# Performance work log

Hardware: AMD Instinct MI355X
Metric: run time of the kernel (lower is better)

## Reference

```python
import jax, jax.numpy as jnp
import numpy as np

T_MIN, T_MAX = 0.6, 1.6
SIM_LO, SIM_HI = 0.5, 0.9
LN_EPS = 1e-5


def _layernorm(x, gamma, beta):
    mu = jnp.mean(x, axis=-1, keepdims=True)
    var = jnp.mean((x - mu) ** 2, axis=-1, keepdims=True)
    return (x - mu) * jax.lax.rsqrt(var + LN_EPS) * gamma + beta


def _cos_sim(a, b, eps=1e-8):
    num = jnp.sum(a * b, axis=-1)
    na = jnp.maximum(jnp.sqrt(jnp.sum(a * a, axis=-1)), eps)
    nb = jnp.maximum(jnp.sqrt(jnp.sum(b * b, axis=-1)), eps)
    return num / (na * nb)


def setup_inputs() -> dict:
    key = jax.random.key(0)
    B, L, D = 2, 4096, 512
    ks = jax.random.split(key, 10)
    s = 0.02
    return {
        "x": jax.random.normal(ks[0], (B, L, D), dtype=jnp.float32),
        "Wq": jax.random.normal(ks[1], (D, D), dtype=jnp.float32) * s,
        "Wk": jax.random.normal(ks[2], (D, D), dtype=jnp.float32) * s,
        "Wv": jax.random.normal(ks[3], (D, D), dtype=jnp.float32) * s,
        "Wp": jax.random.normal(ks[4], (D, D), dtype=jnp.float32) * s,
        "W1": jax.random.normal(ks[5], (4 * D, D), dtype=jnp.float32) * s,
        "b1": jnp.zeros((4 * D,), dtype=jnp.float32),
        "W2": jax.random.normal(ks[6], (D, 4 * D), dtype=jnp.float32) * s,
        "b2": jnp.zeros((D,), dtype=jnp.float32),
        "gamma": jnp.ones((D,), dtype=jnp.float32),
        "beta": jnp.zeros((D,), dtype=jnp.float32),
    }


def reference(x, Wq, Wk, Wv, Wp, W1, b1, W2, b2, gamma, beta):
    B, L, D = x.shape
    xn = _layernorm(x, gamma, beta)
    # TinyAttn with T=1.0, causal=True (torch Linear: x @ W.T)
    Q = jnp.einsum("bld,ed->ble", xn, Wq)
    K = jnp.einsum("bld,ed->ble", xn, Wk)
    V = jnp.einsum("bld,ed->ble", xn, Wv)
    scores = jnp.einsum("bld,bmd->blm", Q, K) / jnp.sqrt(jnp.asarray(D, x.dtype))
    causal = jnp.triu(jnp.ones((L, L), dtype=bool), 1)
    scores = jnp.where(causal, jnp.asarray(-1e30, x.dtype), scores)
    attn = jax.nn.softmax(scores, axis=-1)  # [B, L, L]
    out = jnp.einsum("blm,bmd->bld", attn, V)
    out = jnp.einsum("bld,ed->ble", out, Wp)
    ctx = x + out
    h = _layernorm(ctx, gamma, beta)
    h = jax.nn.gelu(jnp.einsum("bld,fd->blf", h, W1) + b1, approximate=False)
    ctx = ctx + jnp.einsum("blf,df->bld", h, W2) + b2

    # AdaptiveController on last-token attention row
    last_attn = attn[:, -1]  # [B, L]
    p = jnp.clip(last_attn, 1e-9, None)
    H = -jnp.sum(p * jnp.log(p), axis=-1)  # [B]
    Hn = (H - H.min()) / (H.max() - H.min() + 1e-9)
    Hm = jax.lax.stop_gradient(jnp.mean(Hn))  # detached in torch
    T = T_MIN + (T_MAX - T_MIN) * Hm
    sim_th = SIM_HI - (SIM_HI - SIM_LO) * Hm

    # UnconsciousStack: single forward -> stack holds only the just-pushed (K, V), detached.
    q_vec = jnp.mean(Q[:, -1], axis=0, keepdims=True)  # [1, D]
    K_rep = jax.lax.stop_gradient(jnp.mean(K, axis=1))  # [B, D]
    s = jnp.mean(_cos_sim(q_vec, K_rep))  # scalar
    hit = s >= sim_th

    K_cat = jnp.concatenate([K, jax.lax.stop_gradient(K)], axis=1)  # [B, 2L, D]
    V_cat = jnp.concatenate([V, jax.lax.stop_gradient(V)], axis=1)
    scores2 = jnp.einsum("bld,bmd->blm", Q, K_cat) / jnp.sqrt(jnp.asarray(D, x.dtype))
    attn2 = jax.nn.softmax(scores2 / T, axis=-1)  # [B, L, 2L], no causal mask
    reatt = jnp.einsum("blm,bmd->bld", attn2, V_cat)
    ctx = ctx + jnp.where(hit, reatt, jnp.zeros_like(reatt))
    return ctx
```

## Files before the change

kernel.cpp:

```cpp
#include <hip/hip_runtime.h>
#include <math.h>

#define BATCH 2
#define SEQ 4096
#define DIM 512
#define FF 2048
#define NROWS (BATCH*SEQ)
#define KT 32
#define RSQRT_D 0.044194173824159216f

typedef __attribute__((ext_vector_type(8))) short short8;
typedef __attribute__((ext_vector_type(4))) short short4v;
typedef __attribute__((ext_vector_type(4))) float f32x4;

__device__ __forceinline__ float gelu_f(float v) {
    return 0.5f * v * (1.0f + erff(v * 0.70710678118654752440f));
}
__device__ __forceinline__ short bf16b(float x) {
    union { float f; unsigned u; } c; c.f = x;
    unsigned r = (c.u + 0x7FFFu + ((c.u >> 16) & 1u)) >> 16;
    return (short)r;
}
__device__ __forceinline__ float bf16f(short h) {
    union { unsigned u; float f; } c; c.u = ((unsigned)(unsigned short)h) << 16;
    return c.f;
}
__device__ __forceinline__ void gload16(const void* g, void* l) {
    __builtin_amdgcn_global_load_lds(
        (const __attribute__((address_space(1))) unsigned int*)g,
        (__attribute__((address_space(3))) unsigned int*)l, 16, 0, 0);
}
__device__ __forceinline__ float blk_sum256(float v, volatile float* sm) {
    #pragma unroll
    for (int o = 32; o; o >>= 1) v += __shfl_xor(v, o);
    __syncthreads();
    if ((threadIdx.x & 63) == 0) sm[threadIdx.x >> 6] = v;
    __syncthreads();
    return sm[0] + sm[1] + sm[2] + sm[3];
}

__global__ __launch_bounds__(256) void f2bf_all(
        const float* __restrict__ Wq, const float* __restrict__ Wk,
        const float* __restrict__ Wv, const float* __restrict__ Wp,
        const float* __restrict__ W1, const float* __restrict__ W2,
        short* __restrict__ Wcat, short* __restrict__ Wpb,
        short* __restrict__ W1b, short* __restrict__ W2b)
{
    int i = blockIdx.x * 256 + threadIdx.x;
    const float* src; short* dst; int loc;
    if      (i <  32768) { src = Wq; dst = Wcat;          loc = i; }
    else if (i <  65536) { src = Wk; dst = Wcat + 262144; loc = i - 32768; }
    else if (i <  98304) { src = Wv; dst = Wcat + 524288; loc = i - 65536; }
    else if (i < 131072) { src = Wp; dst = Wpb;           loc = i - 98304; }
    else if (i < 262144) { src = W1; dst = W1b;           loc = i - 131072; }
    else                 { src = W2; dst = W2b;           loc = i - 262144; }
    const float4* p = (const float4*)(src + (size_t)loc * 8);
    float4 a = p[0], b = p[1];
    short8 r;
    r[0]=bf16b(a.x); r[1]=bf16b(a.y); r[2]=bf16b(a.z); r[3]=bf16b(a.w);
    r[4]=bf16b(b.x); r[5]=bf16b(b.y); r[6]=bf16b(b.z); r[7]=bf16b(b.w);
    *(short8*)(dst + (size_t)loc * 8) = r;
}

__global__ __launch_bounds__(256) void ln_kernel(const float* __restrict__ x,
        const float* __restrict__ g, const float* __restrict__ be,
        short* __restrict__ o)
{
    int row  = blockIdx.x * 4 + (threadIdx.x >> 6);
    int lane = threadIdx.x & 63;
    const float4* xr = (const float4*)(x + (size_t)row * DIM);
    float4 v0 = xr[lane*2], v1 = xr[lane*2+1];
    float s = v0.x+v0.y+v0.z+v0.w + v1.x+v1.y+v1.z+v1.w;
    #pragma unroll
    for (int off = 32; off; off >>= 1) s += __shfl_xor(s, off);
    float mu = s * (1.0f/DIM);
    float d[8] = {v0.x-mu, v0.y-mu, v0.z-mu, v0.w-mu, v1.x-mu, v1.y-mu, v1.z-mu, v1.w-mu};
    float q = 0.f;
    #pragma unroll
    for (int j = 0; j < 8; ++j) q += d[j]*d[j];
    #pragma unroll
    for (int off = 32; off; off >>= 1) q += __shfl_xor(q, off);
    float rs = rsqrtf(q * (1.0f/DIM) + 1e-5f);
    const float4* g4 = (const float4*)g;
    const float4* b4 = (const float4*)be;
    float4 ga = g4[lane*2], gb = g4[lane*2+1];
    float4 ba = b4[lane*2], bb = b4[lane*2+1];
    float gv[8] = {ga.x,ga.y,ga.z,ga.w, gb.x,gb.y,gb.z,gb.w};
    float bv[8] = {ba.x,ba.y,ba.z,ba.w, bb.x,bb.y,bb.z,bb.w};
    short8 r;
    #pragma unroll
    for (int j = 0; j < 8; ++j) r[j] = bf16b(d[j]*rs*gv[j] + bv[j]);
    *(short8*)(o + (size_t)row * DIM + lane*8) = r;
}

__global__ __launch_bounds__(256) void gemm_v2(
        const short* __restrict__ A, const short* __restrict__ W,
        const float* __restrict__ bias, const float* __restrict__ res,
        float* __restrict__ Cf, short* __restrict__ Cb,
        short* __restrict__ CbK, short* __restrict__ CbV,
        int K, int sa, int sw, int sc, int act, int accum)
{
    __shared__ short As[2][4096];
    __shared__ short Ws[2][4096];
    int tid = threadIdx.x;
    int m0 = blockIdx.y * 128, n0 = blockIdx.x * 128;
    int w = tid >> 6, lane = tid & 63;
    int wr = (w >> 1) * 64, wc = (w & 1) * 64;
    int lr = lane & 15, lg = lane >> 4;
    int srow = tid >> 2, skoff = (tid & 3) * 8;
    const short* Ab = A + (size_t)(m0 + srow) * sa + skoff;
    const short* Wb = W + (size_t)(n0 + srow) * sw + skoff;

    #define STAGE_G(buf, kk) do { \
        gload16(Ab + (kk),                    As[buf] + tid*8); \
        gload16(Ab + (size_t)64*sa + (kk),    As[buf] + 2048 + tid*8); \
        gload16(Wb + (kk),                    Ws[buf] + tid*8); \
        gload16(Wb + (size_t)64*sw + (kk),    Ws[buf] + 2048 + tid*8); } while(0)

    f32x4 acc[4][4];
    f32x4 zero = {0.f, 0.f, 0.f, 0.f};
    #pragma unroll
    for (int i = 0; i < 4; ++i)
        #pragma unroll
        for (int j = 0; j < 4; ++j) acc[i][j] = zero;

    STAGE_G(0, 0);
    __syncthreads();
    int cur = 0;
    for (int k0 = 0; k0 < K; k0 += 32) {
        if (k0 + 32 < K) STAGE_G(cur ^ 1, k0 + 32);
        short8 a[4], b[4];
        #pragma unroll
        for (int i = 0; i < 4; ++i) a[i] = *(const short8*)(As[cur] + (wr + i*16 + lr)*32 + lg*8);
        #pragma unroll
        for (int j = 0; j < 4; ++j) b[j] = *(const short8*)(Ws[cur] + (wc + j*16 + lr)*32 + lg*8);
        #pragma unroll
        for (int i = 0; i < 4; ++i)
            #pragma unroll
            for (int j = 0; j < 4; ++j)
                acc[i][j] = __builtin_amdgcn_mfma_f32_16x16x32_bf16(a[i], b[j], acc[i][j], 0, 0, 0);
        __syncthreads();
        cur ^= 1;
    }
    #undef STAGE_G

    #pragma unroll
    for (int i = 0; i < 4; ++i) {
        #pragma unroll
        for (int r = 0; r < 4; ++r) {
            size_t m = (size_t)m0 + wr + i*16 + lg*4 + r;
            #pragma unroll
            for (int j = 0; j < 4; ++j) {
                int n = n0 + wc + j*16 + lr;
                float v = acc[i][j][r];
                if (bias) v += bias[n];
                if (act)  v = gelu_f(v);
                if (CbK) {
                    int seg = n >> 9, nl = n & 511;
                    short* dst = (seg == 0) ? Cb : (seg == 1) ? CbK : CbV;
                    dst[m * 512 + nl] = bf16b(v);
                } else {
                    if (res) v += res[m * sc + n];
                    size_t idx = m * sc + n;
                    if (Cf) { if (accum) Cf[idx] += v; else Cf[idx] = v; }
                    if (Cb) Cb[idx] = bf16b(v);
                }
            }
        }
    }
}

__global__ __launch_bounds__(256) void vtrans(const short* __restrict__ V,
                                              short* __restrict__ Vt)
{
    __shared__ short t_s[64][72];
    int l0 = blockIdx.x * 64, d0 = blockIdx.y * 64, b = blockIdx.z;
    int t = threadIdx.x;
    const short* src = V + (size_t)b * SEQ * DIM;
    #pragma unroll
    for (int it = 0; it < 2; ++it) {
        int r = (t >> 3) + it * 32, c = (t & 7) * 8;
        *(short8*)&t_s[r][c] = *(const short8*)(src + (size_t)(l0 + r) * DIM + d0 + c);
    }
    __syncthreads();
    short* dst = Vt + (size_t)b * DIM * SEQ;
    #pragma unroll
    for (int it = 0; it < 2; ++it) {
        int r = (t >> 3) + it * 32, c = (t & 7) * 8;
        short8 v;
        #pragma unroll
        for (int j = 0; j < 8; ++j) v[j] = t_s[c + j][r];
        *(short8*)(dst + (size_t)(d0 + r) * SEQ + l0 + c) = v;
    }
}

__global__ __launch_bounds__(512, 2) void attn_v4(
        const short* __restrict__ Q, const short* __restrict__ K,
        const short* __restrict__ Vt, short* __restrict__ Opart,
        float* __restrict__ Mpart, float* __restrict__ Lpart,
        float scale, const float* __restrict__ scale_ptr,
        const float* __restrict__ gate, int causal)
{
    if (gate && gate[0] == 0.0f) return;
    if (scale_ptr) scale = scale_ptr[0];
    extern __shared__ short lds[];
    short* k_s = lds;
    short* v_s = lds + 32768;
    short* p_s = lds + 65536;

    int tid = threadIdx.x, w = tid >> 6, lane = tid & 63;
    int rg = w >> 1, dh = w & 1;
    int lr = lane & 15, lg = lane >> 4;

    int bid = blockIdx.x;
    int cb = bid & 7;
    int c  = cb & 3, b = cb >> 2;
    int ip = bid >> 3;
    int jj0 = ip, jj1 = 63 - ip;
    int TA = causal ? 2*(ip+1)  : 128;
    int TB = causal ? 2*(64-ip) : 128;
    int Ttot = TA + TB;
    int s0 = (Ttot * c) >> 2, s1 = (Ttot * (c+1)) >> 2;

    size_t bofs = (size_t)b * SEQ * DIM;
    size_t vofs = (size_t)b * DIM * SEQ;
    f32x4 zero = {0.f, 0.f, 0.f, 0.f};

    for (int sg = 0; sg < 2; ++sg) {
        int j  = sg ? jj1 : jj0;
        int ta = sg ? (max(s0, TA) - TA) : s0;
        int tb = sg ? (s1 - TA)          : min(s1, TA);
        if (ta >= tb) continue;
        int qw0 = j*64 + rg*16;

        short8 qf[16];
        #pragma unroll
        for (int kc = 0; kc < 16; ++kc)
            qf[kc] = *(const short8*)(Q + bofs + (size_t)(qw0 + lr)*DIM + kc*32 + lg*8);

        f32x4 o[16];
        #pragma unroll
        for (int df = 0; df < 16; ++df) o[df] = zero;
        float mreg[4] = {-1e30f,-1e30f,-1e30f,-1e30f};
        float lreg[4] = {0.f,0.f,0.f,0.f};
        int rowg[4];
        #pragma unroll
        for (int r = 0; r < 4; ++r) rowg[r] = qw0 + lg*4 + r;

        int cur = 0;
        {
            int k0s = ta * KT;
            #pragma unroll
            for (int s4 = 0; s4 < 4; ++s4) {
                int slot = tid + s4*512;
                int row = slot >> 6, cg = slot & 63;
                gload16(K + bofs + (size_t)(k0s + row)*DIM + ((cg ^ (row & 7)) << 3),
                        k_s + slot*8);
                int dpair = slot >> 3, low = slot & 7;
                int d = dpair*2 + (low & 1);
                int kg = (low >> 1) ^ (dpair & 3);
                gload16(Vt + vofs + (size_t)d*SEQ + k0s + kg*8,
                        v_s + slot*8);
            }
        }
        __syncthreads();

        for (int t = ta; t < tb; ++t) {
            int k0 = t * KT;
            if (t + 1 < tb) {
                int k0s = (t + 1) * KT;
                int bo = (cur ^ 1) * 16384;
                #pragma unroll
                for (int s4 = 0; s4 < 4; ++s4) {
                    int slot = tid + s4*512;
                    int row = slot >> 6, cg = slot & 63;
                    gload16(K + bofs + (size_t)(k0s + row)*DIM + ((cg ^ (row & 7)) << 3),
                            k_s + bo + slot*8);
                    int dpair = slot >> 3, low = slot & 7;
                    int d = dpair*2 + (low & 1);
                    int kg = (low >> 1) ^ (dpair & 3);
                    gload16(Vt + vofs + (size_t)d*SEQ + k0s + kg*8,
                            v_s + bo + slot*8);
                }
            }
            f32x4 ss[2];
            ss[0] = zero; ss[1] = zero;
            const short* kb = k_s + cur*16384;
            #pragma unroll
            for (int kc = 0; kc < 16; ++kc) {
                #pragma unroll
                for (int kf = 0; kf < 2; ++kf) {
                    int row = kf*16 + lr;
                    short8 kk = *(const short8*)(kb + row*512 + (((kc*4 + lg) ^ (row & 7)) << 3));
                    ss[kf] = __builtin_amdgcn_mfma_f32_16x16x32_bf16(qf[kc], kk, ss[kf], 0, 0, 0);
                }
            }
            bool needmask = causal && (k0 + KT - 1 > qw0);
            #pragma unroll
            for (int kf = 0; kf < 2; ++kf) {
                int key = k0 + kf*16 + lr;
                #pragma unroll
                for (int r = 0; r < 4; ++r) {
                    float sv = ss[kf][r] * scale;
                    if (needmask && key > rowg[r]) sv = -1e30f;
                    ss[kf][r] = sv;
                }
            }
            float pm[4];
            bool tg = false;
            #pragma unroll
            for (int r = 0; r < 4; ++r) {
                pm[r] = fmaxf(ss[0][r], ss[1][r]);
                tg |= (pm[r] > mreg[r]);
            }
            if (__any(tg)) {
                #pragma unroll
                for (int r = 0; r < 4; ++r) {
                    float v = pm[r];
                    v = fmaxf(v, __shfl_xor(v, 1));
                    v = fmaxf(v, __shfl_xor(v, 2));
                    v = fmaxf(v, __shfl_xor(v, 4));
                    v = fmaxf(v, __shfl_xor(v, 8));
                    float nm = fmaxf(mreg[r], v);
                    float fr = __expf(mreg[r] - nm);
                    mreg[r] = nm;
                    lreg[r] *= fr;
                    #pragma unroll
                    for (int df = 0; df < 16; ++df) o[df][r] *= fr;
                }
            }
            #pragma unroll
            for (int kf = 0; kf < 2; ++kf) {
                #pragma unroll
                for (int r = 0; r < 4; ++r) {
                    float sv = ss[kf][r];
                    float p = (sv < -1e29f) ? 0.0f : __expf(sv - mreg[r]);
                    lreg[r] += p;
                    p_s[w*512 + (lg*4 + r)*32 + kf*16 + lr] = bf16b(p);
                }
            }
            short8 pa = *(const short8*)(p_s + w*512 + lr*32 + lg*8);
            const short* vb = v_s + cur*16384;
            #pragma unroll
            for (int df = 0; df < 16; ++df) {
                int d = dh*256 + df*16 + lr;
                int slot16 = (d >> 1)*8 + (((lg ^ ((d >> 1) & 3)) << 1) | (d & 1));
                short8 vv = *(const short8*)(vb + slot16*8);
                o[df] = __builtin_amdgcn_mfma_f32_16x16x32_bf16(pa, vv, o[df], 0, 0, 0);
            }
            __syncthreads();
            cur ^= 1;
        }

        #pragma unroll
        for (int r = 0; r < 4; ++r) {
            float v = lreg[r];
            v += __shfl_xor(v, 1);
            v += __shfl_xor(v, 2);
            v += __shfl_xor(v, 4);
            v += __shfl_xor(v, 8);
            lreg[r] = v;
        }
        int slot = (b*64 + j)*4 + c;
        size_t obase = ((size_t)slot*8 + w) * 4096;
        #pragma unroll
        for (int df = 0; df < 16; ++df) {
            short4v pk;
            #pragma unroll
            for (int r = 0; r < 4; ++r) pk[r] = bf16b(o[df][r]);
            *(short4v*)(Opart + obase + df*256 + lane*4) = pk;
        }
        if (dh == 0 && lr == 0) {
            #pragma unroll
            for (int r = 0; r < 4; ++r) {
                Mpart[slot*64 + rg*16 + lg*4 + r] = mreg[r];
                Lpart[slot*64 + rg*16 + lg*4 + r] = lreg[r];
            }
        }
    }
}

__global__ __launch_bounds__(256) void attn_merge(
        const short* __restrict__ Opart, const float* __restrict__ Mpart,
        const float* __restrict__ Lpart, short* __restrict__ attb,
        float* __restrict__ outf, const float* __restrict__ gate, int causal)
{
    if (gate && gate[0] == 0.0f) return;
    __shared__ float wts[4][64];
    int j = blockIdx.x, dh = blockIdx.y, b = blockIdx.z;
    int tid = threadIdx.x;
    int ip = (j < 32) ? j : 63 - j;
    int TA = causal ? 2*(ip+1)  : 128;
    int TB = causal ? 2*(64-ip) : 128;
    int Ttot = TA + TB;
    int jstart = (j < 32) ? 0 : TA;
    int jend   = (j < 32) ? TA : Ttot;
    bool val[4];
    #pragma unroll
    for (int c = 0; c < 4; ++c) {
        int sc = (Ttot * c) >> 2, ec = (Ttot * (c+1)) >> 2;
        val[c] = (sc < jend) && (ec > jstart);
    }
    if (tid < 64) {
        float M = -1e30f;
        #pragma unroll
        for (int c = 0; c < 4; ++c)
            if (val[c]) M = fmaxf(M, Mpart[((b*64 + j)*4 + c)*64 + tid]);
        float L = 0.f;
        #pragma unroll
        for (int c = 0; c < 4; ++c)
            if (val[c]) L += Lpart[((b*64 + j)*4 + c)*64 + tid]
                           * __expf(Mpart[((b*64 + j)*4 + c)*64 + tid] - M);
        float invL = 1.0f / L;
        #pragma unroll
        for (int c = 0; c < 4; ++c)
            wts[c][tid] = val[c]
                ? __expf(Mpart[((b*64 + j)*4 + c)*64 + tid] - M) * invL : 0.0f;
    }
    __syncthreads();
    int wv = tid >> 6, lane = tid & 63, lg = lane >> 4, lr = lane & 15;
    int region = wv*2 + dh;
    #pragma unroll 4
    for (int df = 0; df < 16; ++df) {
        float acc[4] = {0.f, 0.f, 0.f, 0.f};
        #pragma unroll
        for (int c = 0; c < 4; ++c) {
            if (!val[c]) continue;
            size_t idx = ((size_t)((b*64 + j)*4 + c)*8 + region)*4096 + df*256 + lane*4;
            short4v v = *(const short4v*)(Opart + idx);
            #pragma unroll
            for (int r = 0; r < 4; ++r)
                acc[r] += wts[c][wv*16 + lg*4 + r] * bf16f(v[r]);
        }
        #pragma unroll
        for (int r = 0; r < 4; ++r) {
            int row = j*64 + wv*16 + lg*4 + r;
            int d = dh*256 + df*16 + lr;
            size_t oidx = (size_t)b*SEQ*DIM + (size_t)row*DIM + d;
            if (attb) attb[oidx] = bf16b(acc[r]);
            else      outf[oidx] += acc[r];
        }
    }
}

__global__ __launch_bounds__(256) void lastrow_scores(const short* __restrict__ Q,
        const short* __restrict__ K, float* __restrict__ slast)
{
    __shared__ float q_l[DIM];
    int b = blockIdx.y;
    int m = blockIdx.x * 256 + threadIdx.x;
    for (int i = threadIdx.x; i < DIM; i += 256)
        q_l[i] = bf16f(Q[((size_t)b*SEQ + SEQ-1)*DIM + i]);
    __syncthreads();
    const short* kr = K + ((size_t)b*SEQ + m) * DIM;
    float s = 0.f;
    for (int d = 0; d < DIM; d += 8) {
        short8 k8 = *(const short8*)(kr + d);
        #pragma unroll
        for (int j = 0; j < 8; ++j) s += q_l[d + j] * bf16f(k8[j]);
    }
    slast[(size_t)b*SEQ + m] = s * RSQRT_D;
}

__global__ __launch_bounds__(256) void entropy_kernel(const float* __restrict__ slast,
        float* __restrict__ H)
{
    __shared__ float sm[4];
    int b = blockIdx.x, t = threadIdx.x;
    const float* s = slast + (size_t)b * SEQ;
    float v[16];
    float mx = -1e30f;
    #pragma unroll
    for (int j = 0; j < 16; ++j) { v[j] = s[t + j*256]; mx = fmaxf(mx, v[j]); }
    #pragma unroll
    for (int o = 32; o; o >>= 1) mx = fmaxf(mx, __shfl_xor(mx, o));
    __syncthreads();
    if ((t & 63) == 0) sm[t >> 6] = mx;
    __syncthreads();
    mx = fmaxf(fmaxf(sm[0], sm[1]), fmaxf(sm[2], sm[3]));
    float se = 0.f;
    #pragma unroll
    for (int j = 0; j < 16; ++j) { v[j] = expf(v[j] - mx); se += v[j]; }
    se = blk_sum256(se, sm);
    float inv = 1.0f / se;
    float h = 0.f;
    #pragma unroll
    for (int j = 0; j < 16; ++j) {
        float p = fmaxf(v[j] * inv, 1e-9f);
        h -= p * logf(p);
    }
    h = blk_sum256(h, sm);
    if (t == 0) H[b] = h;
}

__global__ __launch_bounds__(256) void krep_partial(const short* __restrict__ K,
        float* __restrict__ part)
{
    int b = blockIdx.y, j = blockIdx.x, t = threadIdx.x;
    size_t base = ((size_t)b*SEQ + (size_t)j*64) * DIM;
    float s0 = 0.f, s1 = 0.f;
    for (int r = 0; r < 64; ++r) {
        s0 += bf16f(K[base + (size_t)r*DIM + t]);
        s1 += bf16f(K[base + (size_t)r*DIM + t + 256]);
    }
    size_t o = (size_t)(b*64 + j) * DIM;
    part[o + t] = s0; part[o + t + 256] = s1;
}

__global__ __launch_bounds__(256) void scalar_kernel(const short* __restrict__ Qb,
        const float* __restrict__ part, const float* __restrict__ Hent,
        float* __restrict__ gsc)
{
    __shared__ float sm[4];
    __shared__ float sims[BATCH];
    int t = threadIdx.x;
    float qv0 = 0.5f*(bf16f(Qb[((size_t)0*SEQ + SEQ-1)*DIM + t])     + bf16f(Qb[((size_t)1*SEQ + SEQ-1)*DIM + t]));
    float qv1 = 0.5f*(bf16f(Qb[((size_t)0*SEQ + SEQ-1)*DIM + t+256]) + bf16f(Qb[((size_t)1*SEQ + SEQ-1)*DIM + t+256]));
    for (int b = 0; b < BATCH; ++b) {
        float k0 = 0.f, k1 = 0.f;
        for (int j = 0; j < 64; ++j) {
            k0 += part[(size_t)(b*64+j)*DIM + t];
            k1 += part[(size_t)(b*64+j)*DIM + t + 256];
        }
        k0 *= (1.0f/SEQ); k1 *= (1.0f/SEQ);
        float num = blk_sum256(qv0*k0 + qv1*k1, sm);
        float qq  = blk_sum256(qv0*qv0 + qv1*qv1, sm);
        float kk  = blk_sum256(k0*k0 + k1*k1, sm);
        if (t == 0) {
            float na = fmaxf(sqrtf(qq), 1e-8f);
            float nb = fmaxf(sqrtf(kk), 1e-8f);
            sims[b] = num / (na * nb);
        }
        __syncthreads();
    }
    if (t == 0) {
        float H0 = Hent[0], H1 = Hent[1];
        float mn = fminf(H0, H1), mx = fmaxf(H0, H1);
        float den = (mx - mn) + 1e-9f;
        float Hm = 0.5f*((H0 - mn)/den + (H1 - mn)/den);
        float T  = 0.6f + (1.6f - 0.6f) * Hm;
        float th = 0.9f - (0.9f - 0.5f) * Hm;
        float s  = 0.5f * (sims[0] + sims[1]);
        gsc[0] = (s >= th) ? 1.0f : 0.0f;
        gsc[1] = 1.0f / (sqrtf((float)DIM) * T);
    }
}

extern "C" void kernel_launch(void* const* d_in, const int* in_sizes, int n_in,
                              void* d_out, int out_size, void* d_ws, size_t ws_size,
                              hipStream_t stream)
{
    (void)in_sizes; (void)n_in; (void)out_size; (void)ws_size;
    const float* x     = (const float*)d_in[0];
    const float* Wq    = (const float*)d_in[1];
    const float* Wk    = (const float*)d_in[2];
    const float* Wv    = (const float*)d_in[3];
    const float* Wp    = (const float*)d_in[4];
    const float* W1    = (const float*)d_in[5];
    const float* b1    = (const float*)d_in[6];
    const float* W2    = (const float*)d_in[7];
    const float* b2    = (const float*)d_in[8];
    const float* gamma = (const float*)d_in[9];
    const float* beta  = (const float*)d_in[10];
    float* out = (float*)d_out;

    const size_t NT = (size_t)NROWS * DIM;
    short* bws   = (short*)d_ws;
    short* Qbf   = bws;
    short* Kbf   = Qbf + NT;
    short* Vt    = Kbf + NT;
    short* att   = Vt + NT;
    short* Wcat  = att + NT;
    short* Wpb   = Wcat + 786432;
    short* W1b   = Wpb + 262144;
    short* W2b   = W1b + 1048576;
    float* slast = (float*)(W2b + 1048576);
    float* Hent  = slast + 8192;
    float* kpart = Hent + 8;
    float* gsc   = kpart + 65536;
    float* Mpart = gsc + 8;
    float* Lpart = Mpart + 32768;
    short* xn_bf = (short*)(Lpart + 32768);
    short* h1    = xn_bf + NT;
    short* Opart = xn_bf;

    const int ATTN_LDS = 139264;
    hipFuncSetAttribute((const void*)attn_v4,
                        hipFuncAttributeMaxDynamicSharedMemorySize, ATTN_LDS);

    f2bf_all<<<1536, 256, 0, stream>>>(Wq, Wk, Wv, Wp, W1, W2, Wcat, Wpb, W1b, W2b);

    ln_kernel<<<NROWS/4, 256, 0, stream>>>(x, gamma, beta, xn_bf);

    gemm_v2<<<dim3(1536/128, NROWS/128), 256, 0, stream>>>(
        xn_bf, Wcat, nullptr, nullptr, nullptr, Qbf, Kbf, att,
        DIM, DIM, DIM, DIM, 0, 0);
    vtrans<<<dim3(SEQ/64, DIM/64, BATCH), 256, 0, stream>>>(att, Vt);

    attn_v4<<<256, 512, ATTN_LDS, stream>>>(Qbf, Kbf, Vt, Opart, Mpart, Lpart,
                                            RSQRT_D, nullptr, nullptr, 1);
    attn_merge<<<dim3(64, 2, BATCH), 256, 0, stream>>>(Opart, Mpart, Lpart, att, nullptr,
                                                       nullptr, 1);

    lastrow_scores<<<dim3(SEQ/256, BATCH), 256, 0, stream>>>(Qbf, Kbf, slast);
    entropy_kernel<<<BATCH, 256, 0, stream>>>(slast, Hent);

    gemm_v2<<<dim3(DIM/128, NROWS/128), 256, 0, stream>>>(
        att, Wpb, nullptr, x, out, nullptr, nullptr, nullptr,
        DIM, DIM, DIM, DIM, 0, 0);

    ln_kernel<<<NROWS/4, 256, 0, stream>>>(out, gamma, beta, xn_bf);

    for (int c = 0; c < 2; ++c) {
        gemm_v2<<<dim3(1024/128, NROWS/128), 256, 0, stream>>>(
            xn_bf, W1b + (size_t)c*1024*DIM, b1 + c*1024, nullptr,
            nullptr, h1, nullptr, nullptr,
            DIM, DIM, DIM, 1024, 1, 0);
        gemm_v2<<<dim3(DIM/128, NROWS/128), 256, 0, stream>>>(
            h1, W2b + (size_t)c*1024, (c == 0) ? b2 : nullptr, nullptr,
            out, nullptr, nullptr, nullptr,
            1024, 1024, FF, DIM, 0, 1);
    }

    krep_partial<<<dim3(64, BATCH), 256, 0, stream>>>(Kbf, kpart);
    scalar_kernel<<<1, 256, 0, stream>>>(Qbf, kpart, Hent, gsc);

    attn_v4<<<256, 512, ATTN_LDS, stream>>>(Qbf, Kbf, Vt, Opart, Mpart, Lpart,
                                            0.0f, gsc + 1, gsc, 0);
    attn_merge<<<dim3(64, 2, BATCH), 256, 0, stream>>>(Opart, Mpart, Lpart, nullptr, out,
                                                       gsc, 0);
}
```

Measured before the change: 412.2 us.

## Restructure attention for higher occupancy, split QK over D halves, raise key splits

The attention kernel now splits the QK dot product across the two D-half waves and exchanges bf16 partial scores through LDS. This halves the Q fragments held in registers and switches K/V to single-buffered LDS, which cuts LDS from 136KB to 80KB and lets launch bounds allow 4 blocks per CU. When the workspace is large enough it uses 8 key-range splits instead of 4 and adds swizzled P stores and setprio around the MFMA loops. The GEMM gets a remapped block order and setprio as well. In exchange the scores are rounded to bf16 before the softmax, and the single buffering adds syncs that reduce load/compute overlap.

```diff
diff --git a/kernel.cpp b/kernel.cpp
--- a/kernel.cpp
+++ b/kernel.cpp
@@ -103,7 +103,11 @@
     __shared__ short As[2][4096];
     __shared__ short Ws[2][4096];
     int tid = threadIdx.x;
-    int m0 = blockIdx.y * 128, n0 = blockIdx.x * 128;
+    int nb  = gridDim.x * gridDim.y;
+    int lin = blockIdx.y * gridDim.x + blockIdx.x;
+    int lin2 = (lin & 7) * (nb >> 3) + (lin >> 3);
+    int bx = lin2 % gridDim.x, by = lin2 / gridDim.x;
+    int m0 = by * 128, n0 = bx * 128;
     int w = tid >> 6, lane = tid & 63;
     int wr = (w >> 1) * 64, wc = (w & 1) * 64;
     int lr = lane & 15, lg = lane >> 4;
@@ -134,11 +138,13 @@
         for (int i = 0; i < 4; ++i) a[i] = *(const short8*)(As[cur] + (wr + i*16 + lr)*32 + lg*8);
         #pragma unroll
         for (int j = 0; j < 4; ++j) b[j] = *(const short8*)(Ws[cur] + (wc + j*16 + lr)*32 + lg*8);
+        __builtin_amdgcn_s_setprio(1);
         #pragma unroll
         for (int i = 0; i < 4; ++i)
             #pragma unroll
             for (int j = 0; j < 4; ++j)
                 acc[i][j] = __builtin_amdgcn_mfma_f32_16x16x32_bf16(a[i], b[j], acc[i][j], 0, 0, 0);
+        __builtin_amdgcn_s_setprio(0);
         __syncthreads();
         cur ^= 1;
     }
@@ -194,123 +200,127 @@
     }
 }
 
-__global__ __launch_bounds__(512, 2) void attn_v4(
+__global__ __launch_bounds__(512, 4) void attn_v5(
         const short* __restrict__ Q, const short* __restrict__ K,
         const short* __restrict__ Vt, short* __restrict__ Opart,
         float* __restrict__ Mpart, float* __restrict__ Lpart,
         float scale, const float* __restrict__ scale_ptr,
-        const float* __restrict__ gate, int causal)
+        const float* __restrict__ gate, int causal, int NC, int ncs)
 {
     if (gate && gate[0] == 0.0f) return;
     if (scale_ptr) scale = scale_ptr[0];
     extern __shared__ short lds[];
-    short* k_s = lds;
-    short* v_s = lds + 32768;
-    short* p_s = lds + 65536;
+    short* k_s  = lds;
+    short* v_s  = lds + 16384;
+    short* p_s  = lds + 32768;
+    short* ss_s = lds + 36864;
 
     int tid = threadIdx.x, w = tid >> 6, lane = tid & 63;
     int rg = w >> 1, dh = w & 1;
     int lr = lane & 15, lg = lane >> 4;
 
     int bid = blockIdx.x;
-    int cb = bid & 7;
-    int c  = cb & 3, b = cb >> 2;
-    int ip = bid >> 3;
-    int jj0 = ip, jj1 = 63 - ip;
+    int c  = bid & (NC - 1);
+    int b  = (bid >> ncs) & 1;
+    int ip = bid >> (ncs + 1);
     int TA = causal ? 2*(ip+1)  : 128;
     int TB = causal ? 2*(64-ip) : 128;
     int Ttot = TA + TB;
-    int s0 = (Ttot * c) >> 2, s1 = (Ttot * (c+1)) >> 2;
+    int s0 = (Ttot * c) >> ncs, s1 = (Ttot * (c+1)) >> ncs;
 
     size_t bofs = (size_t)b * SEQ * DIM;
     size_t vofs = (size_t)b * DIM * SEQ;
     f32x4 zero = {0.f, 0.f, 0.f, 0.f};
 
+    int koff[4], voff[4];
+    #pragma unroll
+    for (int i = 0; i < 4; ++i) {
+        int slot = tid + i*512;
+        int row = slot >> 6, cg = slot & 63;
+        koff[i] = row*512 + ((cg ^ (row & 7)) << 3);
+        int dpair = slot >> 3, low = slot & 7;
+        int d = dpair*2 + (low & 1);
+        int kslot = (low >> 1) ^ (dpair & 3);
+        voff[i] = d*SEQ + kslot*8;
+    }
+
     for (int sg = 0; sg < 2; ++sg) {
-        int j  = sg ? jj1 : jj0;
+        int j  = sg ? (63 - ip) : ip;
         int ta = sg ? (max(s0, TA) - TA) : s0;
         int tb = sg ? (s1 - TA)          : min(s1, TA);
         if (ta >= tb) continue;
         int qw0 = j*64 + rg*16;
 
-        short8 qf[16];
-        #pragma unroll
-        for (int kc = 0; kc < 16; ++kc)
-            qf[kc] = *(const short8*)(Q + bofs + (size_t)(qw0 + lr)*DIM + kc*32 + lg*8);
+        short8 qf[8];
+        #pragma unroll
+        for (int kc = 0; kc < 8; ++kc)
+            qf[kc] = *(const short8*)(Q + bofs + (size_t)(qw0 + lr)*DIM
+                                      + dh*256 + kc*32 + lg*8);
 
         f32x4 o[16];
         #pragma unroll
         for (int df = 0; df < 16; ++df) o[df] = zero;
         float mreg[4] = {-1e30f,-1e30f,-1e30f,-1e30f};
         float lreg[4] = {0.f,0.f,0.f,0.f};
-        int rowg[4];
-        #pragma unroll
-        for (int r = 0; r < 4; ++r) rowg[r] = qw0 + lg*4 + r;
-
-        int cur = 0;
-        {
-            int k0s = ta * KT;
-            #pragma unroll
-            for (int s4 = 0; s4 < 4; ++s4) {
-                int slot = tid + s4*512;
-                int row = slot >> 6, cg = slot & 63;
-                gload16(K + bofs + (size_t)(k0s + row)*DIM + ((cg ^ (row & 7)) << 3),
-                        k_s + slot*8);
-                int dpair = slot >> 3, low = slot & 7;
-                int d = dpair*2 + (low & 1);
-                int kg = (low >> 1) ^ (dpair & 3);
-                gload16(Vt + vofs + (size_t)d*SEQ + k0s + kg*8,
-                        v_s + slot*8);
-            }
-        }
+
+        const short* kptr = K + bofs + (size_t)ta * KT * DIM;
+        const short* vptr = Vt + vofs + (size_t)ta * KT;
+        #pragma unroll
+        for (int i = 0; i < 4; ++i) {
+            gload16(kptr + koff[i], k_s + (tid + i*512)*8);
+            gload16(vptr + voff[i], v_s + (tid + i*512)*8);
+        }
+        kptr += KT * DIM;
+        vptr += KT;
         __syncthreads();
 
         for (int t = ta; t < tb; ++t) {
             int k0 = t * KT;
-            if (t + 1 < tb) {
-                int k0s = (t + 1) * KT;
-                int bo = (cur ^ 1) * 16384;
+            bool pre = (t + 1 < tb);
+            f32x4 ss0 = zero, ss1 = zero;
+            __builtin_amdgcn_s_setprio(1);
+            #pragma unroll
+            for (int kc = 0; kc < 8; ++kc) {
+                int g = (dh*32 + kc*4 + lg) ^ (lr & 7);
+                const short* base = k_s + lr*512 + g*8;
+                ss0 = __builtin_amdgcn_mfma_f32_16x16x32_bf16(qf[kc],
+                        *(const short8*)(base), ss0, 0, 0, 0);
+                ss1 = __builtin_amdgcn_mfma_f32_16x16x32_bf16(qf[kc],
+                        *(const short8*)(base + 16*512), ss1, 0, 0, 0);
+            }
+            __builtin_amdgcn_s_setprio(0);
+            short8 pk;
+            #pragma unroll
+            for (int r = 0; r < 4; ++r) { pk[r] = bf16b(ss0[r]); pk[4+r] = bf16b(ss1[r]); }
+            *(short8*)(ss_s + w*512 + lane*8) = pk;
+            __syncthreads();
+            if (pre) {
                 #pragma unroll
-                for (int s4 = 0; s4 < 4; ++s4) {
-                    int slot = tid + s4*512;
-                    int row = slot >> 6, cg = slot & 63;
-                    gload16(K + bofs + (size_t)(k0s + row)*DIM + ((cg ^ (row & 7)) << 3),
-                            k_s + bo + slot*8);
-                    int dpair = slot >> 3, low = slot & 7;
-                    int d = dpair*2 + (low & 1);
-                    int kg = (low >> 1) ^ (dpair & 3);
-                    gload16(Vt + vofs + (size_t)d*SEQ + k0s + kg*8,
-                            v_s + bo + slot*8);
-                }
-            }
-            f32x4 ss[2];
-            ss[0] = zero; ss[1] = zero;
-            const short* kb = k_s + cur*16384;
-            #pragma unroll
-            for (int kc = 0; kc < 16; ++kc) {
+                for (int i = 0; i < 4; ++i)
+                    gload16(kptr + koff[i], k_s + (tid + i*512)*8);
+                kptr += KT * DIM;
+            }
+            short8 po = *(const short8*)(ss_s + (w^1)*512 + lane*8);
+            f32x4 sv[2];
+            #pragma unroll
+            for (int r = 0; r < 4; ++r) {
+                sv[0][r] = (bf16f(pk[r])   + bf16f(po[r]))   * scale;
+                sv[1][r] = (bf16f(pk[4+r]) + bf16f(po[4+r])) * scale;
+            }
+            if (causal && (k0 + KT - 1 > qw0)) {
                 #pragma unroll
                 for (int kf = 0; kf < 2; ++kf) {
-                    int row = kf*16 + lr;
-                    short8 kk = *(const short8*)(kb + row*512 + (((kc*4 + lg) ^ (row & 7)) << 3));
-                    ss[kf] = __builtin_amdgcn_mfma_f32_16x16x32_bf16(qf[kc], kk, ss[kf], 0, 0, 0);
-                }
-            }
-            bool needmask = causal && (k0 + KT - 1 > qw0);
-            #pragma unroll
-            for (int kf = 0; kf < 2; ++kf) {
-                int key = k0 + kf*16 + lr;
-                #pragma unroll
-                for (int r = 0; r < 4; ++r) {
-                    float sv = ss[kf][r] * scale;
-                    if (needmask && key > rowg[r]) sv = -1e30f;
-                    ss[kf][r] = sv;
+                    int key = k0 + kf*16 + lr;
+                    #pragma unroll
+                    for (int r = 0; r < 4; ++r)
+                        if (key > qw0 + lg*4 + r) sv[kf][r] = -1e30f;
                 }
             }
             float pm[4];
             bool tg = false;
             #pragma unroll
             for (int r = 0; r < 4; ++r) {
-                pm[r] = fmaxf(ss[0][r], ss[1][r]);
+                pm[r] = fmaxf(sv[0][r], sv[1][r]);
                 tg |= (pm[r] > mreg[r]);
             }
             if (__any(tg)) {
@@ -333,23 +343,31 @@
             for (int kf = 0; kf < 2; ++kf) {
                 #pragma unroll
                 for (int r = 0; r < 4; ++r) {
-                    float sv = ss[kf][r];
-                    float p = (sv < -1e29f) ? 0.0f : __expf(sv - mreg[r]);
+                    float svv = sv[kf][r];
+                    float p = (svv < -1e29f) ? 0.0f : __expf(svv - mreg[r]);
                     lreg[r] += p;
-                    p_s[w*512 + (lg*4 + r)*32 + kf*16 + lr] = bf16b(p);
+                    int row = lg*4 + r;
+                    int oct = kf*2 + (lr >> 3);
+                    p_s[w*512 + row*32 + ((oct ^ (row & 3)) << 3) + (lr & 7)] = bf16b(p);
                 }
             }
-            short8 pa = *(const short8*)(p_s + w*512 + lr*32 + lg*8);
-            const short* vb = v_s + cur*16384;
+            short8 pa = *(const short8*)(p_s + w*512 + lr*32 + ((lg ^ (lr & 3)) << 3));
+            __builtin_amdgcn_s_setprio(1);
             #pragma unroll
             for (int df = 0; df < 16; ++df) {
                 int d = dh*256 + df*16 + lr;
                 int slot16 = (d >> 1)*8 + (((lg ^ ((d >> 1) & 3)) << 1) | (d & 1));
-                short8 vv = *(const short8*)(vb + slot16*8);
+                short8 vv = *(const short8*)(v_s + slot16*8);
                 o[df] = __builtin_amdgcn_mfma_f32_16x16x32_bf16(pa, vv, o[df], 0, 0, 0);
             }
+            __builtin_amdgcn_s_setprio(0);
             __syncthreads();
-            cur ^= 1;
+            if (pre) {
+                #pragma unroll
+                for (int i = 0; i < 4; ++i)
+                    gload16(vptr + voff[i], v_s + (tid + i*512)*8);
+                vptr += KT;
+            }
         }
 
         #pragma unroll
@@ -361,14 +379,14 @@
             v += __shfl_xor(v, 8);
             lreg[r] = v;
         }
-        int slot = (b*64 + j)*4 + c;
+        int slot = (b*64 + j)*NC + c;
         size_t obase = ((size_t)slot*8 + w) * 4096;
         #pragma unroll
         for (int df = 0; df < 16; ++df) {
-            short4v pk;
-            #pragma unroll
-            for (int r = 0; r < 4; ++r) pk[r] = bf16b(o[df][r]);
-            *(short4v*)(Opart + obase + df*256 + lane*4) = pk;
+            short4v pkk;
+            #pragma unroll
+            for (int r = 0; r < 4; ++r) pkk[r] = bf16b(o[df][r]);
+            *(short4v*)(Opart + obase + df*256 + lane*4) = pkk;
         }
         if (dh == 0 && lr == 0) {
             #pragma unroll
@@ -383,10 +401,11 @@
 __global__ __launch_bounds__(256) void attn_merge(
         const short* __restrict__ Opart, const float* __restrict__ Mpart,
         const float* __restrict__ Lpart, short* __restrict__ attb,
-        float* __restrict__ outf, const float* __restrict__ gate, int causal)
+        float* __restrict__ outf, const float* __restrict__ gate,
+        int causal, int NC, int ncs)
 {
     if (gate && gate[0] == 0.0f) return;
-    __shared__ float wts[4][64];
+    __shared__ float wts[8][64];
     int j = blockIdx.x, dh = blockIdx.y, b = blockIdx.z;
     int tid = threadIdx.x;
     int ip = (j < 32) ? j : 63 - j;
@@ -395,38 +414,32 @@
     int Ttot = TA + TB;
     int jstart = (j < 32) ? 0 : TA;
     int jend   = (j < 32) ? TA : Ttot;
-    bool val[4];
-    #pragma unroll
-    for (int c = 0; c < 4; ++c) {
-        int sc = (Ttot * c) >> 2, ec = (Ttot * (c+1)) >> 2;
-        val[c] = (sc < jend) && (ec > jstart);
+    bool val[8];
+    for (int c = 0; c < 8; ++c) {
+        int sc = (Ttot * c) >> ncs, ec = (Ttot * (c+1)) >> ncs;
+        val[c] = (c < NC) && (sc < jend) && (ec > jstart);
     }
     if (tid < 64) {
         float M = -1e30f;
-        #pragma unroll
-        for (int c = 0; c < 4; ++c)
-            if (val[c]) M = fmaxf(M, Mpart[((b*64 + j)*4 + c)*64 + tid]);
+        for (int c = 0; c < NC; ++c)
+            if (val[c]) M = fmaxf(M, Mpart[((b*64 + j)*NC + c)*64 + tid]);
         float L = 0.f;
-        #pragma unroll
-        for (int c = 0; c < 4; ++c)
-            if (val[c]) L += Lpart[((b*64 + j)*4 + c)*64 + tid]
-                           * __expf(Mpart[((b*64 + j)*4 + c)*64 + tid] - M);
+        for (int c = 0; c < NC; ++c)
+            if (val[c]) L += Lpart[((b*64 + j)*NC + c)*64 + tid]
+                           * __expf(Mpart[((b*64 + j)*NC + c)*64 + tid] - M);
         float invL = 1.0f / L;
-        #pragma unroll
-        for (int c = 0; c < 4; ++c)
+        for (int c = 0; c < NC; ++c)
             wts[c][tid] = val[c]
-                ? __expf(Mpart[((b*64 + j)*4 + c)*64 + tid] - M) * invL : 0.0f;
+                ? __expf(Mpart[((b*64 + j)*NC + c)*64 + tid] - M) * invL : 0.0f;
     }
     __syncthreads();
     int wv = tid >> 6, lane = tid & 63, lg = lane >> 4, lr = lane & 15;
     int region = wv*2 + dh;
-    #pragma unroll 4
     for (int df = 0; df < 16; ++df) {
         float acc[4] = {0.f, 0.f, 0.f, 0.f};
-        #pragma unroll
-        for (int c = 0; c < 4; ++c) {
+        for (int c = 0; c < NC; ++c) {
             if (!val[c]) continue;
-            size_t idx = ((size_t)((b*64 + j)*4 + c)*8 + region)*4096 + df*256 + lane*4;
+            size_t idx = ((size_t)((b*64 + j)*NC + c)*8 + region)*4096 + df*256 + lane*4;
             short4v v = *(const short4v*)(Opart + idx);
             #pragma unroll
             for (int r = 0; r < 4; ++r)
@@ -550,7 +563,7 @@
                               void* d_out, int out_size, void* d_ws, size_t ws_size,
                               hipStream_t stream)
 {
-    (void)in_sizes; (void)n_in; (void)out_size; (void)ws_size;
+    (void)in_sizes; (void)n_in; (void)out_size;
     const float* x     = (const float*)d_in[0];
     const float* Wq    = (const float*)d_in[1];
     const float* Wk    = (const float*)d_in[2];
@@ -578,14 +591,22 @@
     float* Hent  = slast + 8192;
     float* kpart = Hent + 8;
     float* gsc   = kpart + 65536;
+
+    float* Mpart8 = gsc + 8;
+    size_t ml8 = (size_t)128 * 8 * 64;
+    short* xn8 = (short*)(Mpart8 + 2*ml8);
+    size_t opart8_end = ((size_t)(xn8 - bws)) + (size_t)1024 * 8 * 4096;
+    int NC = (ws_size >= opart8_end * 2 + 1024) ? 8 : 4;
+    int ncs = (NC == 8) ? 3 : 2;
+    size_t mlsz = (size_t)128 * NC * 64;
     float* Mpart = gsc + 8;
-    float* Lpart = Mpart + 32768;
-    short* xn_bf = (short*)(Lpart + 32768);
+    float* Lpart = Mpart + mlsz;
+    short* xn_bf = (short*)(Lpart + mlsz);
     short* h1    = xn_bf + NT;
     short* Opart = xn_bf;
 
-    const int ATTN_LDS = 139264;
-    hipFuncSetAttribute((const void*)attn_v4,
+    const int ATTN_LDS = 81920;
+    hipFuncSetAttribute((const void*)attn_v5,
                         hipFuncAttributeMaxDynamicSharedMemorySize, ATTN_LDS);
 
     f2bf_all<<<1536, 256, 0, stream>>>(Wq, Wk, Wv, Wp, W1, W2, Wcat, Wpb, W1b, W2b);
@@ -597,10 +618,10 @@
         DIM, DIM, DIM, DIM, 0, 0);
     vtrans<<<dim3(SEQ/64, DIM/64, BATCH), 256, 0, stream>>>(att, Vt);
 
-    attn_v4<<<256, 512, ATTN_LDS, stream>>>(Qbf, Kbf, Vt, Opart, Mpart, Lpart,
-                                            RSQRT_D, nullptr, nullptr, 1);
+    attn_v5<<<64*NC, 512, ATTN_LDS, stream>>>(Qbf, Kbf, Vt, Opart, Mpart, Lpart,
+                                              RSQRT_D, nullptr, nullptr, 1, NC, ncs);
     attn_merge<<<dim3(64, 2, BATCH), 256, 0, stream>>>(Opart, Mpart, Lpart, att, nullptr,
-                                                       nullptr, 1);
+                                                       nullptr, 1, NC, ncs);
 
     lastrow_scores<<<dim3(SEQ/256, BATCH), 256, 0, stream>>>(Qbf, Kbf, slast);
     entropy_kernel<<<BATCH, 256, 0, stream>>>(slast, Hent);
@@ -625,8 +646,8 @@
     krep_partial<<<dim3(64, BATCH), 256, 0, stream>>>(Kbf, kpart);
     scalar_kernel<<<1, 256, 0, stream>>>(Qbf, kpart, Hent, gsc);
 
-    attn_v4<<<256, 512, ATTN_LDS, stream>>>(Qbf, Kbf, Vt, Opart, Mpart, Lpart,
-                                            0.0f, gsc + 1, gsc, 0);
+    attn_v5<<<64*NC, 512, ATTN_LDS, stream>>>(Qbf, Kbf, Vt, Opart, Mpart, Lpart,
+                                              0.0f, gsc + 1, gsc, 0, NC, ncs);
     attn_merge<<<dim3(64, 2, BATCH), 256, 0, stream>>>(Opart, Mpart, Lpart, nullptr, out,
-                                                       gsc, 0);
-}
+                                                       gsc, 0, NC, ncs);
+}
```

After: 570.2 us. 38.3% more time.

## Split attention across more KV chunks, lazy rescale, swizzle P tile, fuse FFN

Applied to the files above, without the earlier changes.

When the workspace is large enough, the attention kernel splits each query-pair's key range into 8 chunks instead of 4, so 512 blocks launch instead of 256 and the merge kernel combines 8 partials. The online-softmax rescale now fires only when the new max exceeds the running max by more than 8, which skips most O-accumulator rescales but lets exponents grow up to e^8 before renormalising. The P staging tile in LDS gets an XOR swizzle to reduce bank conflicts. The FFN runs as one full-width GEMM pair instead of two halves when the workspace allows it.

```diff
diff --git a/kernel.cpp b/kernel.cpp
--- a/kernel.cpp
+++ b/kernel.cpp
@@ -199,7 +199,7 @@
         const short* __restrict__ Vt, short* __restrict__ Opart,
         float* __restrict__ Mpart, float* __restrict__ Lpart,
         float scale, const float* __restrict__ scale_ptr,
-        const float* __restrict__ gate, int causal)
+        const float* __restrict__ gate, int causal, int NC, int ncs)
 {
     if (gate && gate[0] == 0.0f) return;
     if (scale_ptr) scale = scale_ptr[0];
@@ -213,14 +213,14 @@
     int lr = lane & 15, lg = lane >> 4;
 
     int bid = blockIdx.x;
-    int cb = bid & 7;
-    int c  = cb & 3, b = cb >> 2;
-    int ip = bid >> 3;
+    int c  = bid & (NC - 1);
+    int b  = (bid >> ncs) & 1;
+    int ip = bid >> (ncs + 1);
     int jj0 = ip, jj1 = 63 - ip;
     int TA = causal ? 2*(ip+1)  : 128;
     int TB = causal ? 2*(64-ip) : 128;
     int Ttot = TA + TB;
-    int s0 = (Ttot * c) >> 2, s1 = (Ttot * (c+1)) >> 2;
+    int s0 = (Ttot * c) >> ncs, s1 = (Ttot * (c+1)) >> ncs;
 
     size_t bofs = (size_t)b * SEQ * DIM;
     size_t vofs = (size_t)b * DIM * SEQ;
@@ -311,7 +311,7 @@
             #pragma unroll
             for (int r = 0; r < 4; ++r) {
                 pm[r] = fmaxf(ss[0][r], ss[1][r]);
-                tg |= (pm[r] > mreg[r]);
+                tg |= (pm[r] > mreg[r] + 8.0f);
             }
             if (__any(tg)) {
                 #pragma unroll
@@ -336,10 +336,12 @@
                     float sv = ss[kf][r];
                     float p = (sv < -1e29f) ? 0.0f : __expf(sv - mreg[r]);
                     lreg[r] += p;
-                    p_s[w*512 + (lg*4 + r)*32 + kf*16 + lr] = bf16b(p);
+                    int row = lg*4 + r;
+                    int oct = kf*2 + (lr >> 3);
+                    p_s[w*512 + row*32 + ((oct ^ (row & 3)) << 3) + (lr & 7)] = bf16b(p);
                 }
             }
-            short8 pa = *(const short8*)(p_s + w*512 + lr*32 + lg*8);
+            short8 pa = *(const short8*)(p_s + w*512 + lr*32 + ((lg ^ (lr & 3)) << 3));
             const short* vb = v_s + cur*16384;
             #pragma unroll
             for (int df = 0; df < 16; ++df) {
@@ -361,7 +363,7 @@
             v += __shfl_xor(v, 8);
             lreg[r] = v;
         }
-        int slot = (b*64 + j)*4 + c;
+        int slot = (b*64 + j)*NC + c;
         size_t obase = ((size_t)slot*8 + w) * 4096;
         #pragma unroll
         for (int df = 0; df < 16; ++df) {
@@ -383,10 +385,11 @@
 __global__ __launch_bounds__(256) void attn_merge(
         const short* __restrict__ Opart, const float* __restrict__ Mpart,
         const float* __restrict__ Lpart, short* __restrict__ attb,
-        float* __restrict__ outf, const float* __restrict__ gate, int causal)
+        float* __restrict__ outf, const float* __restrict__ gate,
+        int causal, int NC, int ncs)
 {
     if (gate && gate[0] == 0.0f) return;
-    __shared__ float wts[4][64];
+    __shared__ float wts[8][64];
     int j = blockIdx.x, dh = blockIdx.y, b = blockIdx.z;
     int tid = threadIdx.x;
     int ip = (j < 32) ? j : 63 - j;
@@ -395,38 +398,32 @@
     int Ttot = TA + TB;
     int jstart = (j < 32) ? 0 : TA;
     int jend   = (j < 32) ? TA : Ttot;
-    bool val[4];
-    #pragma unroll
-    for (int c = 0; c < 4; ++c) {
-        int sc = (Ttot * c) >> 2, ec = (Ttot * (c+1)) >> 2;
-        val[c] = (sc < jend) && (ec > jstart);
+    bool val[8];
+    for (int c = 0; c < 8; ++c) {
+        int sc = (Ttot * c) >> ncs, ec = (Ttot * (c+1)) >> ncs;
+        val[c] = (c < NC) && (sc < jend) && (ec > jstart);
     }
     if (tid < 64) {
         float M = -1e30f;
-        #pragma unroll
-        for (int c = 0; c < 4; ++c)
-            if (val[c]) M = fmaxf(M, Mpart[((b*64 + j)*4 + c)*64 + tid]);
+        for (int c = 0; c < NC; ++c)
+            if (val[c]) M = fmaxf(M, Mpart[((b*64 + j)*NC + c)*64 + tid]);
         float L = 0.f;
-        #pragma unroll
-        for (int c = 0; c < 4; ++c)
-            if (val[c]) L += Lpart[((b*64 + j)*4 + c)*64 + tid]
-                           * __expf(Mpart[((b*64 + j)*4 + c)*64 + tid] - M);
+        for (int c = 0; c < NC; ++c)
+            if (val[c]) L += Lpart[((b*64 + j)*NC + c)*64 + tid]
+                           * __expf(Mpart[((b*64 + j)*NC + c)*64 + tid] - M);
         float invL = 1.0f / L;
-        #pragma unroll
-        for (int c = 0; c < 4; ++c)
+        for (int c = 0; c < NC; ++c)
             wts[c][tid] = val[c]
-                ? __expf(Mpart[((b*64 + j)*4 + c)*64 + tid] - M) * invL : 0.0f;
+                ? __expf(Mpart[((b*64 + j)*NC + c)*64 + tid] - M) * invL : 0.0f;
     }
     __syncthreads();
     int wv = tid >> 6, lane = tid & 63, lg = lane >> 4, lr = lane & 15;
     int region = wv*2 + dh;
-    #pragma unroll 4
     for (int df = 0; df < 16; ++df) {
         float acc[4] = {0.f, 0.f, 0.f, 0.f};
-        #pragma unroll
-        for (int c = 0; c < 4; ++c) {
+        for (int c = 0; c < NC; ++c) {
             if (!val[c]) continue;
-            size_t idx = ((size_t)((b*64 + j)*4 + c)*8 + region)*4096 + df*256 + lane*4;
+            size_t idx = ((size_t)((b*64 + j)*NC + c)*8 + region)*4096 + df*256 + lane*4;
             short4v v = *(const short4v*)(Opart + idx);
             #pragma unroll
             for (int r = 0; r < 4; ++r)
@@ -550,7 +547,7 @@
                               void* d_out, int out_size, void* d_ws, size_t ws_size,
                               hipStream_t stream)
 {
-    (void)in_sizes; (void)n_in; (void)out_size; (void)ws_size;
+    (void)in_sizes; (void)n_in; (void)out_size;
     const float* x     = (const float*)d_in[0];
     const float* Wq    = (const float*)d_in[1];
     const float* Wk    = (const float*)d_in[2];
@@ -578,11 +575,22 @@
     float* Hent  = slast + 8192;
     float* kpart = Hent + 8;
     float* gsc   = kpart + 65536;
+
+    float* Mpart8 = gsc + 8;
+    size_t ml8 = (size_t)128 * 8 * 64;
+    short* xn8 = (short*)(Mpart8 + 2*ml8);
+    size_t opart8_end = ((size_t)(xn8 - bws)) + (size_t)1024 * 8 * 4096;
+    int NC = (ws_size >= opart8_end * 2 + 1024) ? 8 : 4;
+    int ncs = (NC == 8) ? 3 : 2;
+    size_t mlsz = (size_t)128 * NC * 64;
     float* Mpart = gsc + 8;
-    float* Lpart = Mpart + 32768;
-    short* xn_bf = (short*)(Lpart + 32768);
+    float* Lpart = Mpart + mlsz;
+    short* xn_bf = (short*)(Lpart + mlsz);
     short* h1    = xn_bf + NT;
     short* Opart = xn_bf;
+
+    size_t ffn_full_end = ((size_t)(h1 - bws) + (size_t)NROWS * FF) * 2;
+    int ffn_full = (ws_size >= ffn_full_end + 1024);
 
     const int ATTN_LDS = 139264;
     hipFuncSetAttribute((const void*)attn_v4,
@@ -597,10 +605,10 @@
         DIM, DIM, DIM, DIM, 0, 0);
     vtrans<<<dim3(SEQ/64, DIM/64, BATCH), 256, 0, stream>>>(att, Vt);
 
-    attn_v4<<<256, 512, ATTN_LDS, stream>>>(Qbf, Kbf, Vt, Opart, Mpart, Lpart,
-                                            RSQRT_D, nullptr, nullptr, 1);
+    attn_v4<<<64*NC, 512, ATTN_LDS, stream>>>(Qbf, Kbf, Vt, Opart, Mpart, Lpart,
+                                              RSQRT_D, nullptr, nullptr, 1, NC, ncs);
     attn_merge<<<dim3(64, 2, BATCH), 256, 0, stream>>>(Opart, Mpart, Lpart, att, nullptr,
-                                                       nullptr, 1);
+                                                       nullptr, 1, NC, ncs);
 
     lastrow_scores<<<dim3(SEQ/256, BATCH), 256, 0, stream>>>(Qbf, Kbf, slast);
     entropy_kernel<<<BATCH, 256, 0, stream>>>(slast, Hent);
@@ -611,22 +619,31 @@
 
     ln_kernel<<<NROWS/4, 256, 0, stream>>>(out, gamma, beta, xn_bf);
 
-    for (int c = 0; c < 2; ++c) {
-        gemm_v2<<<dim3(1024/128, NROWS/128), 256, 0, stream>>>(
-            xn_bf, W1b + (size_t)c*1024*DIM, b1 + c*1024, nullptr,
-            nullptr, h1, nullptr, nullptr,
-            DIM, DIM, DIM, 1024, 1, 0);
+    if (ffn_full) {
+        gemm_v2<<<dim3(FF/128, NROWS/128), 256, 0, stream>>>(
+            xn_bf, W1b, b1, nullptr, nullptr, h1, nullptr, nullptr,
+            DIM, DIM, DIM, FF, 1, 0);
         gemm_v2<<<dim3(DIM/128, NROWS/128), 256, 0, stream>>>(
-            h1, W2b + (size_t)c*1024, (c == 0) ? b2 : nullptr, nullptr,
-            out, nullptr, nullptr, nullptr,
-            1024, 1024, FF, DIM, 0, 1);
+            h1, W2b, b2, nullptr, out, nullptr, nullptr, nullptr,
+            FF, FF, FF, DIM, 0, 1);
+    } else {
+        for (int c = 0; c < 2; ++c) {
+            gemm_v2<<<dim3(1024/128, NROWS/128), 256, 0, stream>>>(
+                xn_bf, W1b + (size_t)c*1024*DIM, b1 + c*1024, nullptr,
+                nullptr, h1, nullptr, nullptr,
+                DIM, DIM, DIM, 1024, 1, 0);
+            gemm_v2<<<dim3(DIM/128, NROWS/128), 256, 0, stream>>>(
+                h1, W2b + (size_t)c*1024, (c == 0) ? b2 : nullptr, nullptr,
+                out, nullptr, nullptr, nullptr,
+                1024, 1024, FF, DIM, 0, 1);
+        }
     }
 
     krep_partial<<<dim3(64, BATCH), 256, 0, stream>>>(Kbf, kpart);
     scalar_kernel<<<1, 256, 0, stream>>>(Qbf, kpart, Hent, gsc);
 
-    attn_v4<<<256, 512, ATTN_LDS, stream>>>(Qbf, Kbf, Vt, Opart, Mpart, Lpart,
-                                            0.0f, gsc + 1, gsc, 0);
+    attn_v4<<<64*NC, 512, ATTN_LDS, stream>>>(Qbf, Kbf, Vt, Opart, Mpart, Lpart,
+                                              0.0f, gsc + 1, gsc, 0, NC, ncs);
     attn_merge<<<dim3(64, 2, BATCH), 256, 0, stream>>>(Opart, Mpart, Lpart, nullptr, out,
-                                                       gsc, 0);
-}
+                                                       gsc, 0, NC, ncs);
+}
```

Measured after the change: 404.3 us. About the same (-1.9%).
